# Performance work log

Hardware: AMD Instinct MI355X
Metric: run time of the kernel (lower is better)

## Reference

```python
import jax, jax.numpy as jnp
import numpy as np

E = 16          # num_experts
D_FULL = 1024   # full_feature_dim
DM = 128        # expert_dim
S = D_FULL // E # per-expert feature slice = 64
P = 2048        # num patches
B = 8
C = 256
W = 3           # local_window (neighbor experts)
DEPTH = 8       # cantor_depth
NEG = -1e9


def _cantor_coord(pos, max_len, depth):
    x = pos / max(1, max_len - 1)
    x = max(1e-6, min(x, 1.0 - 1e-6))
    val, factor = 0.0, 0.5
    for _ in range(depth):
        x *= 3.0
        d = int(x)
        x -= d
        if d == 2:
            val += factor
        factor *= 0.5
    return val


def _expert_routes():
    coords = np.array([_cantor_coord(i, E, DEPTH) for i in range(E)], dtype=np.float32)
    return np.stack([np.argsort(np.abs(coords - coords[i]), kind='stable')[:W] for i in range(E)]).astype(np.int32)


ROUTES = _expert_routes()  # [E, W] static routing table


def setup_inputs():
    key = jax.random.key(0)
    ks = jax.random.split(key, 8)
    h = S // 4
    lim = float(np.sqrt(6.0 / (S + DM)))  # xavier_uniform bound
    penta = jax.random.normal(ks[5], (E, 5, DM), jnp.float32) * 0.02
    penta = penta / jnp.linalg.norm(penta, axis=-1, keepdims=True)
    return {
        'tokens': jax.random.normal(ks[0], (B, P, D_FULL), jnp.float32),
        'fingerprints': jax.random.uniform(ks[1], (P,), jnp.float32),
        'alpha': jnp.ones((E,), jnp.float32),
        'gate_w1': jax.random.normal(ks[2], (E, S, h), jnp.float32) * 0.05,
        'gate_b1': jnp.zeros((E, h), jnp.float32),
        'gate_w2': jax.random.normal(ks[3], (E, h, 1), jnp.float32) * 0.05,
        'gate_b2': jnp.zeros((E, 1), jnp.float32),
        'q_w': jax.random.uniform(ks[4], (E, S, DM), jnp.float32, -lim, lim),
        'k_w': jax.random.uniform(ks[6], (E, S, DM), jnp.float32, -lim, lim),
        'v_w': jax.random.uniform(ks[7], (E, S, DM), jnp.float32, -lim, lim),
        'penta': penta,
        'fusion_w': jnp.ones((5,), jnp.float32) / 5.0,
        'temperature': jnp.float32(0.5),
    }


def _dispatch(fingerprints):
    # Fingerprint band masks, then fixed-capacity gather (static shapes for jit).
    masks = []
    for e in range(E):
        lo, hi = e / E, (e + 1) / E
        m = (fingerprints >= lo) & ((fingerprints <= hi) if e == E - 1 else (fingerprints < hi))
        masks.append(m)
    masks = jnp.stack(masks)                             # [E, P]
    order = jnp.argsort(jnp.where(masks, 0, 1), axis=1)  # stable: assigned patches first
    idx = order[:, :C]                                   # [E, C]
    valid = jnp.take_along_axis(masks, idx, axis=1)      # [E, C]
    return idx, valid


def _forward(tokens, fingerprints, alpha, gate_w1, gate_b1, gate_w2, gate_b2,
             q_w, k_w, v_w, penta, fusion_w, temperature):
    idx, valid = _dispatch(fingerprints)
    Kaff, Qaff, Vs = [], [], []
    for e in range(E):  # fixed structural loop over experts
        feats = tokens[:, idx[e], e * S:(e + 1) * S]                       # [B, C, S]
        g = jax.nn.sigmoid(jax.nn.gelu(feats @ gate_w1[e] + gate_b1[e]) @ gate_w2[e] + gate_b2[e])
        aw = jax.nn.sigmoid(alpha[e])
        feats = feats * (g * aw + (1.0 - aw))                              # gated features
        Q = feats @ q_w[e]
        K = feats @ k_w[e]
        V = feats @ v_w[e]                                                 # [B, C, DM]
        dirs = penta[e] / jnp.linalg.norm(penta[e], axis=-1, keepdims=True)  # [5, DM]
        Kaff.append(jnp.einsum('bcd,vd->vbc', K, dirs))
        Qaff.append(jnp.einsum('bcd,vd->vbc', Q, dirs))
        Vs.append(V)
    Kaff = jnp.stack(Kaff)   # [E, 5, B, C]
    Qaff = jnp.stack(Qaff)   # [E, 5, B, C]
    Vs = jnp.stack(Vs)       # [E, B, C, DM]
    wdir = jax.nn.softmax(fusion_w)
    vmask = valid.astype(jnp.float32)
    out = jnp.zeros((B, P, DM), jnp.float32)
    for e in range(E):
        nb = ROUTES[e]                                  # static [W]
        Knb, Vnb, vnb = Kaff[nb], Vs[nb], vmask[nb]     # [W,5,B,C], [W,B,C,DM], [W,C]
        scores = jnp.einsum('vbi,nvbj->vbinj', Qaff[e], Knb) / temperature
        scores = jnp.where(vnb[None, None, None, :, :] > 0, scores, NEG)
        attn = jax.nn.softmax(scores.reshape(5, B, C, W * C), axis=-1).reshape(5, B, C, W, C)
        att = jnp.einsum('vbinj,nbjd->vbid', attn, Vnb)  # per-direction attended values
        out_e = jnp.einsum('v,vbid->bid', wdir, att) * vmask[e][None, :, None]
        out = out.at[:, idx[e]].add(out_e)              # scatter back to patch positions
    return out


def reference(tokens, fingerprints, alpha, gate_w1, gate_b1, gate_w2, gate_b2,
              q_w, k_w, v_w, penta, fusion_w, temperature):
    return _forward(tokens, fingerprints, alpha, gate_w1, gate_b1, gate_w2, gate_b2,
                    q_w, k_w, v_w, penta, fusion_w, temperature)
```

## Files before the change

### kernel.cpp

```cpp
#include <hip/hip_runtime.h>
#include <cfloat>
#include <math.h>

#define E 16
#define DFULL 1024
#define DM 128
#define S 64
#define P 2048
#define B 8
#define C 256
#define W 3
#define H 16
#define RQ 16
#define NCH 16
#define LOG2E 1.4426950408889634f
#define WST 272

typedef __attribute__((ext_vector_type(8))) short short8;
typedef __attribute__((ext_vector_type(4))) short short4v;
typedef __attribute__((ext_vector_type(4))) float f32x4;
#define MFMA_BF16(a, b, c) __builtin_amdgcn_mfma_f32_16x16x32_bf16((a), (b), (c), 0, 0, 0)

#if defined(__HIP_DEVICE_COMPILE__) && __has_builtin(__builtin_amdgcn_exp2f)
#define EXP2(x) __builtin_amdgcn_exp2f(x)
#else
#define EXP2(x) exp2f(x)
#endif

struct RoutesArg { int nb[E][W]; };

static void compute_routes(int r[E][W]) {
  float coords[E];
  for (int i = 0; i < E; ++i) {
    double x = (double)i / (double)(E - 1);
    if (x < 1e-06) x = 1e-06;
    if (x > 1.0 - 1e-06) x = 1.0 - 1e-06;
    double val = 0.0, factor = 0.5;
    for (int k = 0; k < 8; ++k) {
      x *= 3.0;
      int d = (int)x;
      x -= (double)d;
      if (d == 2) val += factor;
      factor *= 0.5;
    }
    coords[i] = (float)val;
  }
  for (int e = 0; e < E; ++e) {
    float de[E];
    for (int i = 0; i < E; ++i) de[i] = fabsf(coords[i] - coords[e]);
    bool used[E] = {false};
    for (int w = 0; w < W; ++w) {
      int best = -1; float bd = FLT_MAX;
      for (int i = 0; i < E; ++i)
        if (!used[i] && de[i] < bd) { bd = de[i]; best = i; }
      used[best] = true;
      r[e][w] = best;
    }
  }
}

__device__ __forceinline__ unsigned short bfhi(float x) {
  return (unsigned short)(__float_as_uint(x) >> 16);
}
__device__ __forceinline__ float bf2f(unsigned short h) {
  return __uint_as_float(((unsigned)h) << 16);
}
__device__ __forceinline__ float gelu_tanh(float x) {
  float u = 0.7978845608028654f * (x + 0.044715f * x * x * x);
  float ez = __expf(2.0f * u);
  float th = 1.0f - __fdividef(2.0f, ez + 1.0f);
  return 0.5f * x * (1.0f + th);
}
__device__ __forceinline__ float sigmoidf_(float x) {
  return __fdividef(1.0f, 1.0f + __expf(-x));
}

__global__ __launch_bounds__(256) void k_setup(
    const float* __restrict__ fp, const float* __restrict__ qw,
    const float* __restrict__ kw, const float* __restrict__ penta,
    const float* __restrict__ temp, const float* __restrict__ vw,
    int* __restrict__ idx, int* __restrict__ counts,
    unsigned short* __restrict__ qkdT_h, unsigned short* __restrict__ qkdT_l,
    unsigned short* __restrict__ vwT_h, unsigned short* __restrict__ vwT_l) {
  int e = blockIdx.x, t = threadIdx.x;
  __shared__ float s_tr[DM * 65];
  if (blockIdx.y == 1) {
    const float* vwe = vw + (size_t)e * S * DM;
    for (int u = t; u < S * DM; u += 256) {
      int s = u >> 7, d = u & 127;
      s_tr[d * 65 + s] = vwe[u];
    }
    __syncthreads();
    for (int u = t; u < S * DM; u += 256) {
      int d = u >> 6, s = u & 63;
      float f = s_tr[d * 65 + s];
      unsigned short h = bfhi(f), l = bfhi(f - bf2f(h));
      vwT_h[(size_t)e * 8192 + u] = h;
      vwT_l[(size_t)e * 8192 + u] = l;
    }
    return;
  }
  {
    float lo = (float)e * 0.0625f, hi = (float)(e + 1) * 0.0625f;
    bool last = (e == E - 1);
    int p0 = t * 8;
    int m[8]; int ls = 0;
    #pragma unroll
    for (int k = 0; k < 8; ++k) {
      float f = fp[p0 + k];
      bool mm = (f >= lo) && (last ? (f <= hi) : (f < hi));
      m[k] = mm ? 1 : 0;
      ls += m[k];
    }
    __shared__ int sc[256];
    sc[t] = ls;
    __syncthreads();
    for (int o = 1; o < 256; o <<= 1) {
      int v = (t >= o) ? sc[t - o] : 0;
      __syncthreads();
      sc[t] += v;
      __syncthreads();
    }
    int incl = sc[t];
    int M = sc[255];
    int r = incl - ls;
    #pragma unroll
    for (int k = 0; k < 8; ++k) {
      if (m[k]) {
        if (r < C) idx[e * C + r] = p0 + k;
        r++;
      }
    }
    if (t == 0) counts[e] = (M < C) ? M : C;
  }
  __syncthreads();
  __shared__ float s_rn[5];
  if (t < 5) {
    const float* pv = penta + (e * 5 + t) * DM;
    float ss = 0.f;
    for (int d = 0; d < DM; ++d) ss += pv[d] * pv[d];
    s_rn[t] = 1.0f / sqrtf(ss);
  }
  __syncthreads();
  float invT = 1.0f / temp[0];
  int s = t & 63, cg = t >> 6;
  for (int c = cg; c < 10; c += 4) {
    int v = c % 5;
    bool isq = (c < 5);
    const float* wrow = (isq ? qw : kw) + ((size_t)e * S + s) * DM;
    const float* pv = penta + (e * 5 + v) * DM;
    float acc = 0.f;
    #pragma unroll
    for (int d4 = 0; d4 < DM / 4; ++d4) {
      float4 a = ((const float4*)wrow)[d4];
      float4 p = ((const float4*)pv)[d4];
      acc += a.x * p.x + a.y * p.y + a.z * p.z + a.w * p.w;
    }
    float val = acc * s_rn[v] * (isq ? invT : 1.0f);
    unsigned short h = bfhi(val), l = bfhi(val - bf2f(h));
    qkdT_h[(e * 16 + c) * 64 + s] = h;
    qkdT_l[(e * 16 + c) * 64 + s] = l;
  }
  for (int c = 10 + cg; c < 16; c += 4) {
    qkdT_h[(e * 16 + c) * 64 + s] = 0;
    qkdT_l[(e * 16 + c) * 64 + s] = 0;
  }
}

__global__ __launch_bounds__(512, 8) void k_p1(
    const float* __restrict__ tokens, const float* __restrict__ alpha,
    const float* __restrict__ gw1, const float* __restrict__ gb1,
    const float* __restrict__ gw2, const float* __restrict__ gb2,
    const unsigned short* __restrict__ qkdT_h, const unsigned short* __restrict__ qkdT_l,
    const unsigned short* __restrict__ vwT_h, const unsigned short* __restrict__ vwT_l,
    const int* __restrict__ idx, const int* __restrict__ counts,
    float* __restrict__ Qa, float* __restrict__ Ka,
    unsigned short* __restrict__ Vt_h, unsigned short* __restrict__ Vt_l,
    float* __restrict__ kmx, float* __restrict__ kmn,
    float* __restrict__ out) {
  int e = blockIdx.x, b = blockIdx.y, rq = blockIdx.z;
  int t = threadIdx.x;

  {
    int blk = (e * B + b) * NCH + rq;
    if (t < 256) {
      float4 z4 = {0.f, 0.f, 0.f, 0.f};
      ((float4*)out)[(size_t)blk * 256 + t] = z4;
    }
  }

  int Me = counts[e];
  int r0 = rq * RQ;
  if (r0 >= Me) {
    if (t < 5) {
      kmx[((e * 5 + t) * B + b) * NCH + rq] = -FLT_MAX;
      kmn[((e * 5 + t) * B + b) * NCH + rq] = FLT_MAX;
    }
    return;
  }

  __shared__ float s_f[RQ * 65];
  __shared__ __align__(16) unsigned short s_fh[RQ * 72];
  __shared__ __align__(16) unsigned short s_fl[RQ * 72];
  __shared__ float s_gw1[S * H];
  __shared__ float s_gh[RQ * 8 * H];
  __shared__ float s_scl[RQ];
  __shared__ float s_kx[5 * RQ], s_kn[5 * RQ];
  __shared__ __align__(16) unsigned short s_vth[DM * 16];
  __shared__ __align__(16) unsigned short s_vtl[DM * 16];

  if (t < 256) {
    int row = t >> 4, q4 = t & 15;
    int ii = r0 + row;
    int pos = (ii < Me) ? idx[e * C + ii] : idx[e * C];
    const float* trow = tokens + ((size_t)b * P + pos) * DFULL + e * S;
    float4 v4 = ((const float4*)trow)[q4];
    s_f[row * 65 + q4 * 4 + 0] = v4.x;
    s_f[row * 65 + q4 * 4 + 1] = v4.y;
    s_f[row * 65 + q4 * 4 + 2] = v4.z;
    s_f[row * 65 + q4 * 4 + 3] = v4.w;
    ((float4*)s_gw1)[t] = ((const float4*)(gw1 + (size_t)e * S * H))[t];
  }
  __syncthreads();

  if (t < 128) {
    int row = t >> 3, sq = t & 7;
    float hh[H];
    #pragma unroll
    for (int j = 0; j < H; ++j) hh[j] = 0.f;
    #pragma unroll
    for (int k = 0; k < 8; ++k) {
      int s = sq * 8 + k;
      float fs = s_f[row * 65 + s];
      const float* gr = s_gw1 + s * H;
      #pragma unroll
      for (int j = 0; j < H; ++j) hh[j] += fs * gr[j];
    }
    #pragma unroll
    for (int j = 0; j < H; ++j) s_gh[(row * 8 + sq) * H + j] = hh[j];
  }
  __syncthreads();
  if (t < RQ) {
    float z = gb2[e];
    #pragma unroll
    for (int j = 0; j < H; ++j) {
      float hj = gb1[e * H + j];
      #pragma unroll
      for (int p = 0; p < 8; ++p) hj += s_gh[(t * 8 + p) * H + j];
      z += gelu_tanh(hj) * gw2[e * H + j];
    }
    float aw = sigmoidf_(alpha[e]);
    s_scl[t] = sigmoidf_(z) * aw + (1.0f - aw);
  }
  __syncthreads();
  if (t < 256) {
    int row = t >> 4, s0 = (t & 15) * 4;
    float sc = s_scl[row];
    #pragma unroll
    for (int k = 0; k < 4; ++k) {
      float f = s_f[row * 65 + s0 + k] * sc;
      unsigned short h = bfhi(f), l = bfhi(f - bf2f(h));
      s_fh[row * 72 + s0 + k] = h;
      s_fl[row * 72 + s0 + k] = l;
    }
  }
  __syncthreads();

  int L = t & 63, wv = t >> 6, quad = L >> 4, col = L & 15;

  {
    const unsigned short* vTh = vwT_h + (size_t)e * 8192;
    const unsigned short* vTl = vwT_l + (size_t)e * 8192;
    f32x4 va = {0.f, 0.f, 0.f, 0.f};
    int d0 = wv * 16 + col;
    #pragma unroll
    for (int kc = 0; kc < 2; ++kc) {
      int ko = kc * 32 + quad * 8;
      short8 ah = *(const short8*)(s_fh + col * 72 + ko);
      short8 al = *(const short8*)(s_fl + col * 72 + ko);
      short8 bh = *(const short8*)(vTh + d0 * 64 + ko);
      short8 bl = *(const short8*)(vTl + d0 * 64 + ko);
      va = MFMA_BF16(ah, bh, va);
      va = MFMA_BF16(ah, bl, va);
      va = MFMA_BF16(al, bh, va);
    }
    #pragma unroll
    for (int reg = 0; reg < 4; ++reg) {
      int row = quad * 4 + reg;
      float f0 = va[reg];
      unsigned short h0 = bfhi(f0), l0 = bfhi(f0 - bf2f(h0));
      s_vth[d0 * 16 + row] = h0;
      s_vtl[d0 * 16 + row] = l0;
    }
  }

  if (wv == 0) {
    const unsigned short* qTh = qkdT_h + e * 16 * 64;
    const unsigned short* qTl = qkdT_l + e * 16 * 64;
    f32x4 qa = {0.f, 0.f, 0.f, 0.f};
    #pragma unroll
    for (int kc = 0; kc < 2; ++kc) {
      int ko = kc * 32 + quad * 8;
      short8 ah = *(const short8*)(s_fh + col * 72 + ko);
      short8 al = *(const short8*)(s_fl + col * 72 + ko);
      short8 bh = *(const short8*)(qTh + col * 64 + ko);
      short8 bl = *(const short8*)(qTl + col * 64 + ko);
      qa = MFMA_BF16(ah, bh, qa);
      qa = MFMA_BF16(ah, bl, qa);
      qa = MFMA_BF16(al, bh, qa);
    }
    #pragma unroll
    for (int reg = 0; reg < 4; ++reg) {
      int row = quad * 4 + reg;
      int ii = r0 + row;
      float val = qa[reg];
      if (col < 5) {
        if (ii < Me) Qa[((e * 5 + col) * B + b) * C + ii] = val;
      } else if (col < 10) {
        int v = col - 5;
        if (ii < Me) Ka[((e * 5 + v) * B + b) * C + ii] = val;
        s_kx[v * RQ + row] = (ii < Me) ? val : -FLT_MAX;
        s_kn[v * RQ + row] = (ii < Me) ? val : FLT_MAX;
      }
    }
  }
  __syncthreads();
  if (t < 5) {
    float mx = -FLT_MAX, mn = FLT_MAX;
    for (int r = 0; r < RQ; ++r) {
      mx = fmaxf(mx, s_kx[t * RQ + r]);
      mn = fminf(mn, s_kn[t * RQ + r]);
    }
    kmx[((e * 5 + t) * B + b) * NCH + rq] = mx;
    kmn[((e * 5 + t) * B + b) * NCH + rq] = mn;
  }
  if (t < 256) {
    size_t base = (size_t)(e * B + b) * (DM * C);
    int jsl = t >> 7, d = t & 127;
    size_t dst = base + ((size_t)(rq * 2 + jsl) * DM + d) * 8;
    int src = d * 16 + jsl * 8;
    *(short8*)(Vt_h + dst) = *(const short8*)(s_vth + src);
    *(short8*)(Vt_l + dst) = *(const short8*)(s_vtl + src);
  }
}

__global__ __launch_bounds__(512, 8) void k_p2v(
    const float* __restrict__ Qa, const float* __restrict__ Ka,
    const unsigned short* __restrict__ Vt_h, const unsigned short* __restrict__ Vt_l,
    const float* __restrict__ kmx, const float* __restrict__ kmn,
    const int* __restrict__ idx, const int* __restrict__ counts,
    const float* __restrict__ fusw, float* __restrict__ out, RoutesArg R) {
  int e = blockIdx.x, b = blockIdx.y, rq = blockIdx.z;
  int t = threadIdx.x;
  int Me = counts[e];
  int r0 = rq * RQ;
  if (r0 >= Me) return;

  __shared__ __align__(16) float s_ka[3 * 5 * C];
  __shared__ __align__(16) unsigned short s_wh[RQ * WST];
  __shared__ __align__(16) unsigned short s_wl[RQ * WST];
  __shared__ float s_lp[8 * 5 * RQ];
  __shared__ float s_KX[5], s_KN[5];
  __shared__ float s_l[5 * RQ];

  int nbs[3] = {R.nb[e][0], R.nb[e][1], R.nb[e][2]};
  int Mns[3] = {counts[nbs[0]], counts[nbs[1]], counts[nbs[2]]};
  int row = t & 15, jq = t >> 4;
  int ii = r0 + row;
  int L = t & 63, wv = t >> 6, quad = L >> 4, col = L & 15;

  for (int u = t; u < 960; u += 512) {
    int n = (u >= 640) ? 2 : ((u >= 320) ? 1 : 0);
    int r2 = u - n * 320;
    int v = r2 >> 6, off = r2 & 63;
    ((float4*)s_ka)[n * 320 + (v << 6) + off] =
        ((const float4*)(Ka + (((size_t)nbs[n] * 5 + v) * B + b) * C))[off];
  }
  if (wv < 5) {
    float KX = -FLT_MAX, KN = FLT_MAX;
    if (L < 48) {
      int n = L >> 4, k = L & 15;
      int base = ((nbs[n] * 5 + wv) * B + b) * NCH + k;
      KX = kmx[base];
      KN = kmn[base];
    }
    #pragma unroll
    for (int off = 32; off; off >>= 1) {
      KX = fmaxf(KX, __shfl_xor(KX, off));
      KN = fminf(KN, __shfl_xor(KN, off));
    }
    if (L == 0) { s_KX[wv] = KX; s_KN[wv] = KN; }
  }
  __syncthreads();

  float q2[5], m2[5];
  #pragma unroll
  for (int v = 0; v < 5; ++v) {
    float qv = Qa[(((size_t)e * 5 + v) * B + b) * C + ii];
    q2[v] = qv * LOG2E;
    m2[v] = ((qv > 0.f) ? qv * s_KX[v] : qv * s_KN[v]) * LOG2E;
  }

  float lp[5] = {0.f, 0.f, 0.f, 0.f, 0.f};
  for (int n = 0; n < 3; ++n) {
    const float* ka_n = s_ka + n * 1280;
    int Mn = Mns[n];
    for (int j = jq; j < Mn; j += 32) {
      #pragma unroll
      for (int v = 0; v < 5; ++v)
        lp[v] += EXP2(fmaf(q2[v], ka_n[v * C + j], -m2[v]));
    }
  }
  #pragma unroll
  for (int v = 0; v < 5; ++v) {
    lp[v] += __shfl_xor(lp[v], 16);
    lp[v] += __shfl_xor(lp[v], 32);
  }
  if (L < 16) {
    #pragma unroll
    for (int v = 0; v < 5; ++v) s_lp[(wv * 5 + v) * RQ + L] = lp[v];
  }
  __syncthreads();
  if (t < 80) {
    int v = t >> 4, rw = t & 15;
    float l = 0.f;
    #pragma unroll
    for (int w = 0; w < 8; ++w) l += s_lp[(w * 5 + v) * RQ + rw];
    s_l[v * RQ + rw] = l;
  }
  __syncthreads();

  float fw[5];
  #pragma unroll
  for (int v = 0; v < 5; ++v) fw[v] = fusw[v];
  float fmx = fw[0];
  #pragma unroll
  for (int v = 1; v < 5; ++v) fmx = fmaxf(fmx, fw[v]);
  float fsum = 0.f;
  #pragma unroll
  for (int v = 0; v < 5; ++v) { fw[v] = __expf(fw[v] - fmx); fsum += fw[v]; }
  float rfs = __fdividef(1.0f, fsum);
  float c2[5];
  #pragma unroll
  for (int v = 0; v < 5; ++v) {
    float cl = __fdividef(fw[v] * rfs, s_l[v * RQ + row]);
    c2[v] = __log2f(cl) - m2[v];
  }

  int d0 = wv * 16 + col;
  f32x4 acc = {0.f, 0.f, 0.f, 0.f};

  for (int n = 0; n < 3; ++n) {
    int ne = nbs[n], Mn = Mns[n];
    int kcN = (Mn + 31) >> 5;
    const float* ka_n = s_ka + n * 1280;
    __syncthreads();
    int jlim = kcN * 32;
    for (int j0 = jq * 4; j0 < jlim; j0 += 128) {
      short4v h4, l4;
      #pragma unroll
      for (int k2 = 0; k2 < 4; ++k2) {
        int jj = j0 + k2;
        float ww = 0.f;
        if (jj < Mn) {
          #pragma unroll
          for (int v = 0; v < 5; ++v)
            ww += EXP2(fmaf(q2[v], ka_n[v * C + jj], c2[v]));
        }
        unsigned short h = bfhi(ww), l = bfhi(ww - bf2f(h));
        h4[k2] = (short)h;
        l4[k2] = (short)l;
      }
      *(short4v*)(s_wh + row * WST + j0) = h4;
      *(short4v*)(s_wl + row * WST + j0) = l4;
    }
    __syncthreads();
    const unsigned short* vbh = Vt_h + (size_t)(ne * B + b) * (DM * C);
    const unsigned short* vbl = Vt_l + (size_t)(ne * B + b) * (DM * C);
    size_t sb0 = ((size_t)quad * DM + d0) * 8;
    short8 bh = *(const short8*)(vbh + sb0);
    short8 bl = *(const short8*)(vbl + sb0);
    for (int kc = 0; kc < kcN; ++kc) {
      int kn = (kc + 1 < kcN) ? (kc + 1) : kc;
      size_t sb = ((size_t)(kn * 4 + quad) * DM + d0) * 8;
      short8 nbh = *(const short8*)(vbh + sb);
      short8 nbl = *(const short8*)(vbl + sb);
      int ko = kc * 32 + quad * 8;
      short8 ah = *(const short8*)(s_wh + col * WST + ko);
      short8 al = *(const short8*)(s_wl + col * WST + ko);
      acc = MFMA_BF16(ah, bh, acc);
      acc = MFMA_BF16(ah, bl, acc);
      acc = MFMA_BF16(al, bh, acc);
      bh = nbh;
      bl = nbl;
    }
  }

  #pragma unroll
  for (int reg = 0; reg < 4; ++reg) {
    int rr = quad * 4 + reg;
    int iw = r0 + rr;
    if (iw < Me) {
      int pos = idx[e * C + iw];
      out[((size_t)b * P + pos) * DM + d0] = acc[reg];
    }
  }
}

extern "C" void kernel_launch(void* const* d_in, const int* in_sizes, int n_in,
                              void* d_out, int out_size, void* d_ws, size_t ws_size,
                              hipStream_t stream) {
  const float* tokens = (const float*)d_in[0];
  const float* fingerprints = (const float*)d_in[1];
  const float* alpha = (const float*)d_in[2];
  const float* gw1 = (const float*)d_in[3];
  const float* gb1 = (const float*)d_in[4];
  const float* gw2 = (const float*)d_in[5];
  const float* gb2 = (const float*)d_in[6];
  const float* qw = (const float*)d_in[7];
  const float* kw = (const float*)d_in[8];
  const float* vw = (const float*)d_in[9];
  const float* penta = (const float*)d_in[10];
  const float* fusw = (const float*)d_in[11];
  const float* temp = (const float*)d_in[12];
  float* out = (float*)d_out;

  float* ws = (float*)d_ws;
  float* Qa = ws;
  float* Ka = Qa + (size_t)E * 5 * B * C;
  float* kmx = Ka + (size_t)E * 5 * B * C;
  float* kmn = kmx + (size_t)E * 5 * B * NCH;
  unsigned short* qkdT_h = (unsigned short*)(kmn + (size_t)E * 5 * B * NCH);
  unsigned short* qkdT_l = qkdT_h + (size_t)E * 16 * 64;
  unsigned short* vwT_h = qkdT_l + (size_t)E * 16 * 64;
  unsigned short* vwT_l = vwT_h + (size_t)E * S * DM;
  unsigned short* Vt_h = vwT_l + (size_t)E * S * DM;
  unsigned short* Vt_l = Vt_h + (size_t)E * B * DM * C;
  int* idx = (int*)(Vt_l + (size_t)E * B * DM * C);
  int* counts = idx + (size_t)E * C;

  RoutesArg R;
  compute_routes(R.nb);

  k_setup<<<dim3(E, 2), dim3(256), 0, stream>>>(fingerprints, qw, kw, penta, temp, vw,
                                                idx, counts, qkdT_h, qkdT_l, vwT_h, vwT_l);
  k_p1<<<dim3(E, B, NCH), dim3(512), 0, stream>>>(tokens, alpha, gw1, gb1, gw2, gb2,
                                                  qkdT_h, qkdT_l, vwT_h, vwT_l,
                                                  idx, counts, Qa, Ka, Vt_h, Vt_l,
                                                  kmx, kmn, out);
  k_p2v<<<dim3(E, B, NCH), dim3(512), 0, stream>>>(Qa, Ka, Vt_h, Vt_l, kmx, kmn,
                                                   idx, counts, fusw, out, R);
}
```

Baseline: 177.2 us.

## Process 32 query rows per p2v block to reuse V loads across two MFMA tiles

The attention-value kernel now handles 32 query rows per block instead of 16, halving the grid. Each wave computes two 16-row MFMA tiles that share the same V fragments, so global V traffic and the K-staging work per block are amortised over twice as many rows. Along with this, the V prefetch is hoisted before the weight computation, MFMA issue priority is raised, the lp scratch aliases s_wh, and the gate MLP reduction in p1 is parallelised with shuffles and a padded shared layout. The cost is fewer blocks, which may lower occupancy and leave work imbalanced when per-expert counts are small, plus more registers per thread.

```diff
diff --git a/kernel.cpp b/kernel.cpp
--- a/kernel.cpp
+++ b/kernel.cpp
@@ -13,11 +13,12 @@
 #define H 16
 #define RQ 16
 #define NCH 16
+#define RQ2 32
+#define NCH2 8
 #define LOG2E 1.4426950408889634f
 #define WST 272
 
 typedef __attribute__((ext_vector_type(8))) short short8;
-typedef __attribute__((ext_vector_type(4))) short short4v;
 typedef __attribute__((ext_vector_type(4))) float f32x4;
 #define MFMA_BF16(a, b, c) __builtin_amdgcn_mfma_f32_16x16x32_bf16((a), (b), (c), 0, 0, 0)
 
@@ -203,7 +204,7 @@
   __shared__ __align__(16) unsigned short s_fh[RQ * 72];
   __shared__ __align__(16) unsigned short s_fl[RQ * 72];
   __shared__ float s_gw1[S * H];
-  __shared__ float s_gh[RQ * 8 * H];
+  __shared__ float s_gh[RQ * 8 * 17];
   __shared__ float s_scl[RQ];
   __shared__ float s_kx[5 * RQ], s_kn[5 * RQ];
   __shared__ __align__(16) unsigned short s_vth[DM * 16];
@@ -237,20 +238,21 @@
       for (int j = 0; j < H; ++j) hh[j] += fs * gr[j];
     }
     #pragma unroll
-    for (int j = 0; j < H; ++j) s_gh[(row * 8 + sq) * H + j] = hh[j];
-  }
-  __syncthreads();
-  if (t < RQ) {
-    float z = gb2[e];
-    #pragma unroll
-    for (int j = 0; j < H; ++j) {
-      float hj = gb1[e * H + j];
-      #pragma unroll
-      for (int p = 0; p < 8; ++p) hj += s_gh[(t * 8 + p) * H + j];
-      z += gelu_tanh(hj) * gw2[e * H + j];
-    }
-    float aw = sigmoidf_(alpha[e]);
-    s_scl[t] = sigmoidf_(z) * aw + (1.0f - aw);
+    for (int j = 0; j < H; ++j) s_gh[(row * 8 + sq) * 17 + j] = hh[j];
+  }
+  __syncthreads();
+  if (t < 256) {
+    int row = t >> 4, j = t & 15;
+    float hj = gb1[e * H + j];
+    #pragma unroll
+    for (int p = 0; p < 8; ++p) hj += s_gh[(row * 8 + p) * 17 + j];
+    float gz = gelu_tanh(hj) * gw2[e * H + j];
+    #pragma unroll
+    for (int off = 1; off < 16; off <<= 1) gz += __shfl_xor(gz, off);
+    if (j == 0) {
+      float aw = sigmoidf_(alpha[e]);
+      s_scl[row] = sigmoidf_(gb2[e] + gz) * aw + (1.0f - aw);
+    }
   }
   __syncthreads();
   if (t < 256) {
@@ -344,7 +346,7 @@
   }
 }
 
-__global__ __launch_bounds__(512, 8) void k_p2v(
+__global__ __launch_bounds__(512, 6) void k_p2v(
     const float* __restrict__ Qa, const float* __restrict__ Ka,
     const unsigned short* __restrict__ Vt_h, const unsigned short* __restrict__ Vt_l,
     const float* __restrict__ kmx, const float* __restrict__ kmn,
@@ -353,21 +355,29 @@
   int e = blockIdx.x, b = blockIdx.y, rq = blockIdx.z;
   int t = threadIdx.x;
   int Me = counts[e];
-  int r0 = rq * RQ;
+  int r0 = rq * RQ2;
   if (r0 >= Me) return;
 
   __shared__ __align__(16) float s_ka[3 * 5 * C];
-  __shared__ __align__(16) unsigned short s_wh[RQ * WST];
-  __shared__ __align__(16) unsigned short s_wl[RQ * WST];
-  __shared__ float s_lp[8 * 5 * RQ];
+  __shared__ __align__(16) unsigned short s_wh[RQ2 * WST];
+  __shared__ __align__(16) unsigned short s_wl[RQ2 * WST];
+  __shared__ float s_l[5 * RQ2];
   __shared__ float s_KX[5], s_KN[5];
-  __shared__ float s_l[5 * RQ];
+  float* s_lp = (float*)s_wh;
 
   int nbs[3] = {R.nb[e][0], R.nb[e][1], R.nb[e][2]};
   int Mns[3] = {counts[nbs[0]], counts[nbs[1]], counts[nbs[2]]};
-  int row = t & 15, jq = t >> 4;
+  int row = t & 31, jq = t >> 5;
   int ii = r0 + row;
   int L = t & 63, wv = t >> 6, quad = L >> 4, col = L & 15;
+
+  float qv[5];
+  #pragma unroll
+  for (int v = 0; v < 5; ++v)
+    qv[v] = Qa[(((size_t)e * 5 + v) * B + b) * C + ii];
+  float fw[5];
+  #pragma unroll
+  for (int v = 0; v < 5; ++v) fw[v] = fusw[v];
 
   for (int u = t; u < 960; u += 512) {
     int n = (u >= 640) ? 2 : ((u >= 320) ? 1 : 0);
@@ -396,43 +406,36 @@
   float q2[5], m2[5];
   #pragma unroll
   for (int v = 0; v < 5; ++v) {
-    float qv = Qa[(((size_t)e * 5 + v) * B + b) * C + ii];
-    q2[v] = qv * LOG2E;
-    m2[v] = ((qv > 0.f) ? qv * s_KX[v] : qv * s_KN[v]) * LOG2E;
+    q2[v] = qv[v] * LOG2E;
+    m2[v] = ((qv[v] > 0.f) ? qv[v] * s_KX[v] : qv[v] * s_KN[v]) * LOG2E;
   }
 
   float lp[5] = {0.f, 0.f, 0.f, 0.f, 0.f};
   for (int n = 0; n < 3; ++n) {
     const float* ka_n = s_ka + n * 1280;
     int Mn = Mns[n];
-    for (int j = jq; j < Mn; j += 32) {
+    for (int j = jq; j < Mn; j += 16) {
       #pragma unroll
       for (int v = 0; v < 5; ++v)
         lp[v] += EXP2(fmaf(q2[v], ka_n[v * C + j], -m2[v]));
     }
   }
   #pragma unroll
-  for (int v = 0; v < 5; ++v) {
-    lp[v] += __shfl_xor(lp[v], 16);
-    lp[v] += __shfl_xor(lp[v], 32);
-  }
-  if (L < 16) {
-    #pragma unroll
-    for (int v = 0; v < 5; ++v) s_lp[(wv * 5 + v) * RQ + L] = lp[v];
-  }
-  __syncthreads();
-  if (t < 80) {
-    int v = t >> 4, rw = t & 15;
+  for (int v = 0; v < 5; ++v) lp[v] += __shfl_xor(lp[v], 32);
+  if (L < 32) {
+    #pragma unroll
+    for (int v = 0; v < 5; ++v) s_lp[(wv * 5 + v) * RQ2 + L] = lp[v];
+  }
+  __syncthreads();
+  if (t < 160) {
+    int v = t >> 5, rw = t & 31;
     float l = 0.f;
     #pragma unroll
-    for (int w = 0; w < 8; ++w) l += s_lp[(w * 5 + v) * RQ + rw];
-    s_l[v * RQ + rw] = l;
-  }
-  __syncthreads();
-
-  float fw[5];
-  #pragma unroll
-  for (int v = 0; v < 5; ++v) fw[v] = fusw[v];
+    for (int w = 0; w < 8; ++w) l += s_lp[(w * 5 + v) * RQ2 + rw];
+    s_l[v * RQ2 + rw] = l;
+  }
+  __syncthreads();
+
   float fmx = fw[0];
   #pragma unroll
   for (int v = 1; v < 5; ++v) fmx = fmaxf(fmx, fw[v]);
@@ -443,23 +446,29 @@
   float c2[5];
   #pragma unroll
   for (int v = 0; v < 5; ++v) {
-    float cl = __fdividef(fw[v] * rfs, s_l[v * RQ + row]);
+    float cl = __fdividef(fw[v] * rfs, s_l[v * RQ2 + row]);
     c2[v] = __log2f(cl) - m2[v];
   }
 
   int d0 = wv * 16 + col;
-  f32x4 acc = {0.f, 0.f, 0.f, 0.f};
+  f32x4 acc0 = {0.f, 0.f, 0.f, 0.f};
+  f32x4 acc1 = {0.f, 0.f, 0.f, 0.f};
 
   for (int n = 0; n < 3; ++n) {
     int ne = nbs[n], Mn = Mns[n];
     int kcN = (Mn + 31) >> 5;
     const float* ka_n = s_ka + n * 1280;
     __syncthreads();
+    const unsigned short* vbh = Vt_h + (size_t)(ne * B + b) * (DM * C);
+    const unsigned short* vbl = Vt_l + (size_t)(ne * B + b) * (DM * C);
+    size_t sb0 = ((size_t)quad * DM + d0) * 8;
+    short8 bh = *(const short8*)(vbh + sb0);
+    short8 bl = *(const short8*)(vbl + sb0);
     int jlim = kcN * 32;
-    for (int j0 = jq * 4; j0 < jlim; j0 += 128) {
-      short4v h4, l4;
+    for (int j0 = jq * 8; j0 < jlim; j0 += 128) {
+      short8 h8, l8;
       #pragma unroll
-      for (int k2 = 0; k2 < 4; ++k2) {
+      for (int k2 = 0; k2 < 8; ++k2) {
         int jj = j0 + k2;
         float ww = 0.f;
         if (jj < Mn) {
@@ -468,41 +477,47 @@
             ww += EXP2(fmaf(q2[v], ka_n[v * C + jj], c2[v]));
         }
         unsigned short h = bfhi(ww), l = bfhi(ww - bf2f(h));
-        h4[k2] = (short)h;
-        l4[k2] = (short)l;
+        h8[k2] = (short)h;
+        l8[k2] = (short)l;
       }
-      *(short4v*)(s_wh + row * WST + j0) = h4;
-      *(short4v*)(s_wl + row * WST + j0) = l4;
+      *(short8*)(s_wh + row * WST + j0) = h8;
+      *(short8*)(s_wl + row * WST + j0) = l8;
     }
     __syncthreads();
-    const unsigned short* vbh = Vt_h + (size_t)(ne * B + b) * (DM * C);
-    const unsigned short* vbl = Vt_l + (size_t)(ne * B + b) * (DM * C);
-    size_t sb0 = ((size_t)quad * DM + d0) * 8;
-    short8 bh = *(const short8*)(vbh + sb0);
-    short8 bl = *(const short8*)(vbl + sb0);
+    __builtin_amdgcn_s_setprio(1);
     for (int kc = 0; kc < kcN; ++kc) {
       int kn = (kc + 1 < kcN) ? (kc + 1) : kc;
       size_t sb = ((size_t)(kn * 4 + quad) * DM + d0) * 8;
       short8 nbh = *(const short8*)(vbh + sb);
       short8 nbl = *(const short8*)(vbl + sb);
       int ko = kc * 32 + quad * 8;
-      short8 ah = *(const short8*)(s_wh + col * WST + ko);
-      short8 al = *(const short8*)(s_wl + col * WST + ko);
-      acc = MFMA_BF16(ah, bh, acc);
-      acc = MFMA_BF16(ah, bl, acc);
-      acc = MFMA_BF16(al, bh, acc);
+      short8 ah0 = *(const short8*)(s_wh + col * WST + ko);
+      short8 al0 = *(const short8*)(s_wl + col * WST + ko);
+      short8 ah1 = *(const short8*)(s_wh + (16 + col) * WST + ko);
+      short8 al1 = *(const short8*)(s_wl + (16 + col) * WST + ko);
+      acc0 = MFMA_BF16(ah0, bh, acc0);
+      acc1 = MFMA_BF16(ah1, bh, acc1);
+      acc0 = MFMA_BF16(ah0, bl, acc0);
+      acc1 = MFMA_BF16(ah1, bl, acc1);
+      acc0 = MFMA_BF16(al0, bh, acc0);
+      acc1 = MFMA_BF16(al1, bh, acc1);
       bh = nbh;
       bl = nbl;
     }
-  }
-
-  #pragma unroll
-  for (int reg = 0; reg < 4; ++reg) {
-    int rr = quad * 4 + reg;
-    int iw = r0 + rr;
-    if (iw < Me) {
-      int pos = idx[e * C + iw];
-      out[((size_t)b * P + pos) * DM + d0] = acc[reg];
+    __builtin_amdgcn_s_setprio(0);
+  }
+
+  #pragma unroll
+  for (int mt = 0; mt < 2; ++mt) {
+    f32x4 a = mt ? acc1 : acc0;
+    #pragma unroll
+    for (int reg = 0; reg < 4; ++reg) {
+      int rr = mt * 16 + quad * 4 + reg;
+      int iw = r0 + rr;
+      if (iw < Me) {
+        int pos = idx[e * C + iw];
+        out[((size_t)b * P + pos) * DM + d0] = a[reg];
+      }
     }
   }
 }
@@ -548,6 +563,6 @@
                                                   qkdT_h, qkdT_l, vwT_h, vwT_l,
                                                   idx, counts, Qa, Ka, Vt_h, Vt_l,
                                                   kmx, kmn, out);
-  k_p2v<<<dim3(E, B, NCH), dim3(512), 0, stream>>>(Qa, Ka, Vt_h, Vt_l, kmx, kmn,
-                                                   idx, counts, fusw, out, R);
-}
+  k_p2v<<<dim3(E, B, NCH2), dim3(512), 0, stream>>>(Qa, Ka, Vt_h, Vt_l, kmx, kmn,
+                                                    idx, counts, fusw, out, R);
+}
```

Result: faster. 171.5 us (-3.2%).
